# Kernel tuning notes

Measured on AMD Instinct MI355X. Metric: run time of the kernel, lower is better.

The kernel has to match this reference:

```python
import jax, jax.numpy as jnp
import numpy as np

K = 20          # knn neighbors
EPS = 1e-5      # InstanceNorm2d default eps
SLOPE = 0.2     # LeakyReLU negative_slope


def setup_inputs() -> dict:
    key = jax.random.key(0)
    k1, k2 = jax.random.split(key)
    x = jax.random.normal(k1, (4, 3, 8192), dtype=jnp.float32)   # [B, C, N] point cloud
    W = jax.random.normal(k2, (64, 6), dtype=jnp.float32) * 0.05  # 1x1 conv weight [out, 2C], bias=False
    return {"x": x, "W": W}


def reference(x, W):
    B, C, N = x.shape
    # ---- KNN graph: pairwise squared distances + top-k nearest ----
    inner = jnp.einsum('bcn,bcm->bnm', x, x)                 # [B,N,N]
    sq = jnp.sum(x * x, axis=1)                              # [B,N]
    dist = sq[:, :, None] - 2.0 * inner + sq[:, None, :]     # [B,N,N]
    _, idx = jax.lax.top_k(-dist, K)                         # [B,N,K] nearest (incl. self)
    # ---- gather edge features: concat(x_i, x_j - x_i) ----
    xt = jnp.transpose(x, (0, 2, 1))                         # [B,N,C]
    nbr = jax.vmap(lambda pts, i: pts[i])(xt, idx)           # [B,N,K,C]
    ctr = jnp.broadcast_to(xt[:, :, None, :], nbr.shape)     # [B,N,K,C]
    edge = jnp.concatenate([ctr, nbr - ctr], axis=-1)        # [B,N,K,2C]
    # ---- 1x1 conv (no bias) ----
    y = jnp.einsum('bnkc,oc->bonk', edge, W)                 # [B,O,N,K]
    # ---- InstanceNorm2d (affine=False, biased var) ----
    mean = jnp.mean(y, axis=(2, 3), keepdims=True)
    var = jnp.var(y, axis=(2, 3), keepdims=True)
    y = (y - mean) * jax.lax.rsqrt(var + EPS)
    # ---- LeakyReLU(0.2) ----
    y = jnp.where(y >= 0, y, SLOPE * y)
    # ---- max-pool over neighbors ----
    return jnp.max(y, axis=-1)                               # [B,O,N]
```

## Files before the change

### kernel.cpp

```cpp
#include <hip/hip_runtime.h>

#define Nn 8192
#define Bb 4
#define KK 20
#define OO 64
#define EPSF 1e-5f
#define SLOPEF 0.2f

#define NBUCK 56
#define CAP 256
#define BOFF 476
#define CLO 0.00390625f
#define CHI 63.9999961853f
#define XBINS 256
#define XSCALE 25.6f
#define XOFF 5.0f


__global__ __launch_bounds__(1024) void sort_kernel(const float* __restrict__ x,
                                                    float4* __restrict__ sx,
                                                    int* __restrict__ ord,
                                                    int* __restrict__ cumg) {
  __shared__ unsigned hcnt[XBINS];
  __shared__ unsigned base[XBINS];
  __shared__ unsigned char binb[Nn];
  const int b = blockIdx.x;
  const float* xb = x + b * 3 * Nn;
  for (int t = threadIdx.x; t < XBINS; t += 1024) hcnt[t] = 0u;
  __syncthreads();
  for (int j = threadIdx.x; j < Nn; j += 1024) {
    float a0 = xb[j];
    int bin = (int)((a0 + XOFF) * XSCALE);
    bin = bin < 0 ? 0 : (bin > XBINS - 1 ? XBINS - 1 : bin);
    binb[j] = (unsigned char)bin;
    atomicAdd(&hcnt[bin], 1u);
  }
  __syncthreads();
  if (threadIdx.x == 0) {
    unsigned run = 0;
    #pragma unroll 8
    for (int i = 0; i < XBINS; ++i) {
      base[i] = run;
      cumg[b * (XBINS + 1) + i] = (int)run;
      run += hcnt[i];
    }
    cumg[b * (XBINS + 1) + XBINS] = (int)run;
  }
  __syncthreads();
  for (int j = threadIdx.x; j < Nn; j += 1024) {
    float a0 = xb[j], a1 = xb[Nn + j], a2 = xb[2 * Nn + j];
    unsigned slot = atomicAdd(&base[binb[j]], 1u);
    sx[b * Nn + slot] = make_float4(a0, a1, a2, a0 * a0 + a1 * a1 + a2 * a2);
    ord[b * Nn + slot] = j;
  }
}


__global__ __launch_bounds__(256, 8) void knn_kernel(const float4* __restrict__ sx,
                                                     const int* __restrict__ ord,
                                                     const int* __restrict__ cumg,
                                                     int* __restrict__ idx_out) {
  __shared__ unsigned hist[4][64];
  __shared__ unsigned long long cdk[4][CAP];
  __shared__ unsigned ccnt[4];

  const int lane = threadIdx.x & 63;
  const int wid  = threadIdx.x >> 6;
  const int b    = blockIdx.y;
  const int r    = (wid << 11) + blockIdx.x;

  const float4* __restrict__ sxb  = sx + b * Nn;
  const int*    __restrict__ ordb = ord + b * Nn;
  const int*    __restrict__ cumb = cumg + b * (XBINS + 1);
  const float4 me = sxb[r];

  hist[wid][lane] = 0u;
  if (lane == 0) ccnt[wid] = 0u;

  int sub0 = r - 256; sub0 = sub0 < 0 ? 0 : (sub0 > Nn - 512 ? Nn - 512 : sub0);
  #pragma unroll
  for (int i = 0; i < 8; ++i) {
    float4 p = sxb[sub0 + i * 64 + lane];
    float inner = fmaf(p.x, me.x, fmaf(p.y, me.y, p.z * me.z));
    float d  = fmaf(-2.0f, inner, me.w + p.w);
    float dc = __builtin_amdgcn_fmed3f(d, CLO, CHI);
    atomicAdd(&hist[wid][(__float_as_uint(dc) >> 21) - BOFF], 1u);
  }
  unsigned cum = (lane < NBUCK) ? hist[wid][lane] : 0u;
  #pragma unroll
  for (int off = 1; off < 64; off <<= 1) {
    unsigned o = __shfl_up(cum, off);
    if (lane >= off) cum += o;
  }
  int crit = __popcll(__ballot(lane < NBUCK && cum < KK));
  float Tup = (crit >= NBUCK - 1) ? 256.0f
                                  : __uint_as_float((unsigned)(BOFF + crit + 1) << 21);

  float rT = sqrtf(Tup);
  int bn_ = (int)((me.x - rT - 1e-5f + XOFF) * XSCALE);
  bn_ = bn_ < 0 ? 0 : (bn_ > XBINS - 1 ? XBINS - 1 : bn_);
  int rlo = cumb[bn_];
  bn_ = (int)((me.x + rT + 1e-5f + XOFF) * XSCALE);
  bn_ = bn_ < 0 ? 0 : (bn_ > XBINS - 1 ? XBINS - 1 : bn_);
  int rhi = cumb[bn_ + 1];

  for (int j0 = rlo; j0 < rhi; j0 += 256) {
    #pragma unroll
    for (int t = 0; t < 4; ++t) {
      int j = j0 + t * 64 + lane;
      if (j < rhi) {
        float4 p = sxb[j];
        float inner = fmaf(p.x, me.x, fmaf(p.y, me.y, p.z * me.z));
        float d = fmaf(-2.0f, inner, me.w + p.w);
        if (d < Tup) {
          int bb = (int)__float_as_uint(d);
          unsigned sk = (unsigned)(bb ^ ((bb >> 31) | 0x80000000));
          unsigned c = atomicAdd(&ccnt[wid], 1u);
          if (c < CAP)
            cdk[wid][c] = ((unsigned long long)sk << 32) | (unsigned)ordb[j];
        }
      }
    }
  }
  int cnt = (int)ccnt[wid];

  for (int it = 0; cnt > CAP && it < 4; ++it) {
    hist[wid][lane] = 0u;
    const float s56 = 56.0f / Tup;
    for (int j0 = rlo; j0 < rhi; j0 += 64) {
      int j = j0 + lane;
      if (j < rhi) {
        float4 p = sxb[j];
        float inner = fmaf(p.x, me.x, fmaf(p.y, me.y, p.z * me.z));
        float d = fmaf(-2.0f, inner, me.w + p.w);
        int bk = (int)(d * s56);
        if ((unsigned)bk < (unsigned)NBUCK) atomicAdd(&hist[wid][bk], 1u);
      }
    }
    unsigned cum2 = (lane < NBUCK) ? hist[wid][lane] : 0u;
    #pragma unroll
    for (int off = 1; off < 64; off <<= 1) {
      unsigned o = __shfl_up(cum2, off);
      if (lane >= off) cum2 += o;
    }
    int crit2 = __popcll(__ballot(lane < NBUCK && cum2 < KK));
    unsigned cnew = __shfl(cum2, crit2);
    if (cnew <= CAP) {
      if (lane == 0) ccnt[wid] = 0u;
      for (int j0 = rlo; j0 < rhi; j0 += 64) {
        int j = j0 + lane;
        if (j < rhi) {
          float4 p = sxb[j];
          float inner = fmaf(p.x, me.x, fmaf(p.y, me.y, p.z * me.z));
          float d = fmaf(-2.0f, inner, me.w + p.w);
          int bk = (int)(d * s56);
          if (bk <= crit2) {
            int bb = (int)__float_as_uint(d);
            unsigned sk = (unsigned)(bb ^ ((bb >> 31) | 0x80000000));
            unsigned c = atomicAdd(&ccnt[wid], 1u);
            if (c < CAP)
              cdk[wid][c] = ((unsigned long long)sk << 32) | (unsigned)ordb[j];
          }
        }
      }
      cnt = (int)ccnt[wid];
      break;
    }
    Tup = (float)(crit2 + 1) * (Tup / 56.0f);
    rT = sqrtf(Tup);
    bn_ = (int)((me.x - rT - 1e-5f + XOFF) * XSCALE);
    bn_ = bn_ < 0 ? 0 : (bn_ > XBINS - 1 ? XBINS - 1 : bn_);
    rlo = cumb[bn_];
    bn_ = (int)((me.x + rT + 1e-5f + XOFF) * XSCALE);
    bn_ = bn_ < 0 ? 0 : (bn_ > XBINS - 1 ? XBINS - 1 : bn_);
    rhi = cumb[bn_ + 1];
    cnt = (int)cnew;
  }

  const int nOrig = ordb[r];
  int* op = idx_out + (b * Nn + nOrig) * KK;

  if (cnt <= CAP) {
    for (int c = lane; c < cnt; c += 64) {
      unsigned long long key = cdk[wid][c];
      int rank = 0;
      for (int c2 = 0; c2 < cnt; ++c2) rank += (cdk[wid][c2] < key) ? 1 : 0;
      if (rank < KK) op[rank] = (int)(key & 0xFFFFFFFFu);
    }
  } else {
    unsigned long long last = 0ull;
    for (int k = 0; k < KK; ++k) {
      unsigned long long best = ~0ull;
      for (int j0 = rlo; j0 < rhi; j0 += 64) {
        int j = j0 + lane;
        if (j < rhi) {
          float4 p = sxb[j];
          float inner = fmaf(p.x, me.x, fmaf(p.y, me.y, p.z * me.z));
          float d = fmaf(-2.0f, inner, me.w + p.w);
          int bb = (int)__float_as_uint(d);
          unsigned sk = (unsigned)(bb ^ ((bb >> 31) | 0x80000000));
          unsigned long long key = ((unsigned long long)sk << 32) | (unsigned)ordb[j];
          if (key > last && key < best) best = key;
        }
      }
      #pragma unroll
      for (int off = 32; off >= 1; off >>= 1) {
        unsigned lo_ = (unsigned)best, hi_ = (unsigned)(best >> 32);
        unsigned olo = __shfl_xor(lo_, off), ohi = __shfl_xor(hi_, off);
        unsigned long long o = ((unsigned long long)ohi << 32) | olo;
        if (o < best) best = o;
      }
      if (lane == 0) op[k] = (int)(best & 0xFFFFFFFFu);
      last = best;
    }
  }
}


__global__ __launch_bounds__(256) void uv_kernel(const float* __restrict__ x,
                                                 const float* __restrict__ W,
                                                 float* __restrict__ u,
                                                 float* __restrict__ v) {
  int gid = blockIdx.x * 256 + threadIdx.x;
  int o  = gid & 63;
  int bn = gid >> 6;
  int b  = bn >> 13;
  int n  = bn & (Nn - 1);
  const float* xb = x + b * 3 * Nn;
  float x0 = xb[n], x1 = xb[Nn + n], x2 = xb[2 * Nn + n];
  float wa0 = W[o * 6 + 0], wa1 = W[o * 6 + 1], wa2 = W[o * 6 + 2];
  float wb0 = W[o * 6 + 3], wb1 = W[o * 6 + 4], wb2 = W[o * 6 + 5];
  u[gid] = (wa0 - wb0) * x0 + (wa1 - wb1) * x1 + (wa2 - wb2) * x2;
  v[gid] = wb0 * x0 + wb1 * x1 + wb2 * x2;
}


__global__ __launch_bounds__(256) void gather_kernel(const int* __restrict__ idx,
                                                     float* __restrict__ u,
                                                     const float* __restrict__ v,
                                                     float* __restrict__ stats) {
  __shared__ float ls1[4][64], ls2[4][64];
  int b  = blockIdx.y;
  int o  = threadIdx.x & 63;
  int ys = threadIdx.x >> 6;
  const float* vb = v + (size_t)b * Nn * OO;
  float s1 = 0.f, s2 = 0.f;
  for (int i = 0; i < 16; ++i) {
    int n = blockIdx.x * 64 + ys * 16 + i;
    const int* ip = idx + (b * Nn + n) * KK;
    float un = u[(size_t)(b * Nn + n) * OO + o];
    float sv = 0.f, sv2 = 0.f, mv = -__builtin_inff();
    #pragma unroll
    for (int k = 0; k < KK; ++k) {
      int j = ip[k];
      float val = vb[(size_t)j * OO + o];
      sv += val; sv2 += val * val; mv = fmaxf(mv, val);
    }
    u[(size_t)(b * Nn + n) * OO + o] = un + mv;
    s1 += (float)KK * un + sv;
    s2 += (float)KK * un * un + 2.f * un * sv + sv2;
  }
  ls1[ys][o] = s1; ls2[ys][o] = s2;
  __syncthreads();
  if (ys == 0) {
    float t1 = ls1[0][o] + ls1[1][o] + ls1[2][o] + ls1[3][o];
    float t2 = ls2[0][o] + ls2[1][o] + ls2[2][o] + ls2[3][o];
    atomicAdd(&stats[(b * OO + o) * 2 + 0], t1);
    atomicAdd(&stats[(b * OO + o) * 2 + 1], t2);
  }
}


__global__ __launch_bounds__(256) void out_kernel(const float* __restrict__ pm,
                                                  const float* __restrict__ stats,
                                                  float* __restrict__ out) {
  __shared__ float tile[64][65];
  int b  = blockIdx.y;
  int o  = threadIdx.x & 63;
  int ys = threadIdx.x >> 6;
  const float inv_cnt = 1.0f / (float)(Nn * KK);
  float S1 = stats[(b * OO + o) * 2 + 0];
  float S2 = stats[(b * OO + o) * 2 + 1];
  float mean = S1 * inv_cnt;
  float var  = S2 * inv_cnt - mean * mean;
  float istd = rsqrtf(var + EPSF);
  for (int i = 0; i < 16; ++i) {
    int n = blockIdx.x * 64 + ys * 16 + i;
    float val = (pm[(size_t)(b * Nn + n) * OO + o] - mean) * istd;
    val = (val >= 0.f) ? val : SLOPEF * val;
    tile[ys * 16 + i][o] = val;
  }
  __syncthreads();
  int nb = blockIdx.x * 64;
  for (int i = 0; i < 16; ++i) {
    int oo = ys * 16 + i;
    out[(size_t)(b * OO + oo) * Nn + nb + o] = tile[o][oo];
  }
}


extern "C" void kernel_launch(void* const* d_in, const int* in_sizes, int n_in,
                              void* d_out, int out_size, void* d_ws, size_t ws_size,
                              hipStream_t stream) {
  const float* x = (const float*)d_in[0];
  const float* W = (const float*)d_in[1];
  float* out = (float*)d_out;

  char* ws = (char*)d_ws;
  int*    idx   = (int*)ws;
  float*  u     = (float*)(ws + 2621440);
  float*  v     = (float*)(ws + 11010048);
  float*  stats = (float*)(ws + 19398656);
  float4* sx    = (float4*)(ws + 19402752);
  int*    ord   = (int*)(ws + 19927040);
  int*    cumg  = (int*)(ws + 20058112);

  hipMemsetAsync(stats, 0, Bb * OO * 2 * sizeof(float), stream);
  sort_kernel  <<<Bb, 1024, 0, stream>>>(x, sx, ord, cumg);
  uv_kernel    <<<dim3((Bb * Nn * OO) / 256), 256, 0, stream>>>(x, W, u, v);
  knn_kernel   <<<dim3(Nn / 4, Bb), 256, 0, stream>>>(sx, ord, cumg, idx);
  gather_kernel<<<dim3(128, Bb), 256, 0, stream>>>(idx, u, v, stats);
  out_kernel   <<<dim3(128, Bb), 256, 0, stream>>>(u, stats, out);
}
```

Measured before the change: 217.1 us.

## Process four adjacent sorted queries per wavefront sharing candidate loads

Each wavefront now handles four consecutive queries in x-sorted order instead of one. It scans the union of their candidate ranges once, so each loaded point is reused for four distance evaluations, which amortises global loads and loop overhead. The candidate buffer capacity is reduced to fit four per-query buffers in shared memory. In exchange the union range is wider than each query's own range, register pressure rises under the 8-waves launch bound, and the smaller capacity may trigger the slower refinement paths more often.

```diff
diff --git a/kernel.cpp b/kernel.cpp
--- a/kernel.cpp
+++ b/kernel.cpp
@@ -8,7 +8,7 @@
 #define SLOPEF 0.2f
 
 #define NBUCK 56
-#define CAP 256
+#define CAP 120
 #define BOFF 476
 #define CLO 0.00390625f
 #define CHI 63.9999961853f
@@ -60,158 +60,182 @@
                                                      const int* __restrict__ ord,
                                                      const int* __restrict__ cumg,
                                                      int* __restrict__ idx_out) {
-  __shared__ unsigned hist[4][64];
-  __shared__ unsigned long long cdk[4][CAP];
-  __shared__ unsigned ccnt[4];
+  __shared__ unsigned hist[4][4][64];
+  __shared__ unsigned long long cdk[4][4][CAP];
+  __shared__ unsigned ccnt[4][4];
 
   const int lane = threadIdx.x & 63;
   const int wid  = threadIdx.x >> 6;
   const int b    = blockIdx.y;
-  const int r    = (wid << 11) + blockIdx.x;
+  const int g    = (wid << 9) + blockIdx.x;
+  const int r0   = g << 2;
 
   const float4* __restrict__ sxb  = sx + b * Nn;
   const int*    __restrict__ ordb = ord + b * Nn;
   const int*    __restrict__ cumb = cumg + b * (XBINS + 1);
-  const float4 me = sxb[r];
-
-  hist[wid][lane] = 0u;
-  if (lane == 0) ccnt[wid] = 0u;
-
-  int sub0 = r - 256; sub0 = sub0 < 0 ? 0 : (sub0 > Nn - 512 ? Nn - 512 : sub0);
+
+  float4 me[4];
   #pragma unroll
+  for (int q = 0; q < 4; ++q) me[q] = sxb[r0 + q];
+
+  #pragma unroll
+  for (int q = 0; q < 4; ++q) hist[wid][q][lane] = 0u;
+  if (lane < 4) ccnt[wid][lane] = 0u;
+
+  int sub0 = r0 + 2 - 256; sub0 = sub0 < 0 ? 0 : (sub0 > Nn - 512 ? Nn - 512 : sub0);
+  #pragma unroll 2
   for (int i = 0; i < 8; ++i) {
     float4 p = sxb[sub0 + i * 64 + lane];
-    float inner = fmaf(p.x, me.x, fmaf(p.y, me.y, p.z * me.z));
-    float d  = fmaf(-2.0f, inner, me.w + p.w);
-    float dc = __builtin_amdgcn_fmed3f(d, CLO, CHI);
-    atomicAdd(&hist[wid][(__float_as_uint(dc) >> 21) - BOFF], 1u);
-  }
-  unsigned cum = (lane < NBUCK) ? hist[wid][lane] : 0u;
+    #pragma unroll
+    for (int q = 0; q < 4; ++q) {
+      float inner = fmaf(p.x, me[q].x, fmaf(p.y, me[q].y, p.z * me[q].z));
+      float d  = fmaf(-2.0f, inner, me[q].w + p.w);
+      float dc = __builtin_amdgcn_fmed3f(d, CLO, CHI);
+      atomicAdd(&hist[wid][q][(__float_as_uint(dc) >> 21) - BOFF], 1u);
+    }
+  }
+
+  float Tup[4]; int rlo[4], rhi[4];
+  int rloU = Nn, rhiU = 0;
   #pragma unroll
-  for (int off = 1; off < 64; off <<= 1) {
-    unsigned o = __shfl_up(cum, off);
-    if (lane >= off) cum += o;
-  }
-  int crit = __popcll(__ballot(lane < NBUCK && cum < KK));
-  float Tup = (crit >= NBUCK - 1) ? 256.0f
-                                  : __uint_as_float((unsigned)(BOFF + crit + 1) << 21);
-
-  float rT = sqrtf(Tup);
-  int bn_ = (int)((me.x - rT - 1e-5f + XOFF) * XSCALE);
-  bn_ = bn_ < 0 ? 0 : (bn_ > XBINS - 1 ? XBINS - 1 : bn_);
-  int rlo = cumb[bn_];
-  bn_ = (int)((me.x + rT + 1e-5f + XOFF) * XSCALE);
-  bn_ = bn_ < 0 ? 0 : (bn_ > XBINS - 1 ? XBINS - 1 : bn_);
-  int rhi = cumb[bn_ + 1];
-
-  for (int j0 = rlo; j0 < rhi; j0 += 256) {
-    #pragma unroll
-    for (int t = 0; t < 4; ++t) {
-      int j = j0 + t * 64 + lane;
-      if (j < rhi) {
-        float4 p = sxb[j];
-        float inner = fmaf(p.x, me.x, fmaf(p.y, me.y, p.z * me.z));
-        float d = fmaf(-2.0f, inner, me.w + p.w);
-        if (d < Tup) {
-          int bb = (int)__float_as_uint(d);
-          unsigned sk = (unsigned)(bb ^ ((bb >> 31) | 0x80000000));
-          unsigned c = atomicAdd(&ccnt[wid], 1u);
-          if (c < CAP)
-            cdk[wid][c] = ((unsigned long long)sk << 32) | (unsigned)ordb[j];
-        }
-      }
-    }
-  }
-  int cnt = (int)ccnt[wid];
-
-  for (int it = 0; cnt > CAP && it < 4; ++it) {
-    hist[wid][lane] = 0u;
-    const float s56 = 56.0f / Tup;
-    for (int j0 = rlo; j0 < rhi; j0 += 64) {
-      int j = j0 + lane;
-      if (j < rhi) {
-        float4 p = sxb[j];
-        float inner = fmaf(p.x, me.x, fmaf(p.y, me.y, p.z * me.z));
-        float d = fmaf(-2.0f, inner, me.w + p.w);
-        int bk = (int)(d * s56);
-        if ((unsigned)bk < (unsigned)NBUCK) atomicAdd(&hist[wid][bk], 1u);
-      }
-    }
-    unsigned cum2 = (lane < NBUCK) ? hist[wid][lane] : 0u;
+  for (int q = 0; q < 4; ++q) {
+    unsigned cum = (lane < NBUCK) ? hist[wid][q][lane] : 0u;
     #pragma unroll
     for (int off = 1; off < 64; off <<= 1) {
-      unsigned o = __shfl_up(cum2, off);
-      if (lane >= off) cum2 += o;
-    }
-    int crit2 = __popcll(__ballot(lane < NBUCK && cum2 < KK));
-    unsigned cnew = __shfl(cum2, crit2);
-    if (cnew <= CAP) {
-      if (lane == 0) ccnt[wid] = 0u;
-      for (int j0 = rlo; j0 < rhi; j0 += 64) {
-        int j = j0 + lane;
-        if (j < rhi) {
-          float4 p = sxb[j];
-          float inner = fmaf(p.x, me.x, fmaf(p.y, me.y, p.z * me.z));
-          float d = fmaf(-2.0f, inner, me.w + p.w);
-          int bk = (int)(d * s56);
-          if (bk <= crit2) {
+      unsigned o = __shfl_up(cum, off);
+      if (lane >= off) cum += o;
+    }
+    int crit = __popcll(__ballot(lane < NBUCK && cum < KK));
+    Tup[q] = (crit >= NBUCK - 1) ? 256.0f
+                                 : __uint_as_float((unsigned)(BOFF + crit + 1) << 21);
+    float rT = sqrtf(Tup[q]);
+    int bn_ = (int)((me[q].x - rT - 1e-5f + XOFF) * XSCALE);
+    bn_ = bn_ < 0 ? 0 : (bn_ > XBINS - 1 ? XBINS - 1 : bn_);
+    rlo[q] = cumb[bn_];
+    bn_ = (int)((me[q].x + rT + 1e-5f + XOFF) * XSCALE);
+    bn_ = bn_ < 0 ? 0 : (bn_ > XBINS - 1 ? XBINS - 1 : bn_);
+    rhi[q] = cumb[bn_ + 1];
+    rloU = rlo[q] < rloU ? rlo[q] : rloU;
+    rhiU = rhi[q] > rhiU ? rhi[q] : rhiU;
+  }
+
+  for (int j0 = rloU; j0 < rhiU; j0 += 128) {
+    #pragma unroll
+    for (int t = 0; t < 2; ++t) {
+      int j = j0 + t * 64 + lane;
+      if (j < rhiU) {
+        float4 p = sxb[j];
+        #pragma unroll
+        for (int q = 0; q < 4; ++q) {
+          float inner = fmaf(p.x, me[q].x, fmaf(p.y, me[q].y, p.z * me[q].z));
+          float d = fmaf(-2.0f, inner, me[q].w + p.w);
+          if (d < Tup[q]) {
             int bb = (int)__float_as_uint(d);
             unsigned sk = (unsigned)(bb ^ ((bb >> 31) | 0x80000000));
-            unsigned c = atomicAdd(&ccnt[wid], 1u);
+            unsigned c = atomicAdd(&ccnt[wid][q], 1u);
             if (c < CAP)
-              cdk[wid][c] = ((unsigned long long)sk << 32) | (unsigned)ordb[j];
+              cdk[wid][q][c] = ((unsigned long long)sk << 32) | (unsigned)ordb[j];
           }
         }
       }
-      cnt = (int)ccnt[wid];
-      break;
-    }
-    Tup = (float)(crit2 + 1) * (Tup / 56.0f);
-    rT = sqrtf(Tup);
-    bn_ = (int)((me.x - rT - 1e-5f + XOFF) * XSCALE);
-    bn_ = bn_ < 0 ? 0 : (bn_ > XBINS - 1 ? XBINS - 1 : bn_);
-    rlo = cumb[bn_];
-    bn_ = (int)((me.x + rT + 1e-5f + XOFF) * XSCALE);
-    bn_ = bn_ < 0 ? 0 : (bn_ > XBINS - 1 ? XBINS - 1 : bn_);
-    rhi = cumb[bn_ + 1];
-    cnt = (int)cnew;
-  }
-
-  const int nOrig = ordb[r];
-  int* op = idx_out + (b * Nn + nOrig) * KK;
-
-  if (cnt <= CAP) {
-    for (int c = lane; c < cnt; c += 64) {
-      unsigned long long key = cdk[wid][c];
-      int rank = 0;
-      for (int c2 = 0; c2 < cnt; ++c2) rank += (cdk[wid][c2] < key) ? 1 : 0;
-      if (rank < KK) op[rank] = (int)(key & 0xFFFFFFFFu);
-    }
-  } else {
-    unsigned long long last = 0ull;
-    for (int k = 0; k < KK; ++k) {
-      unsigned long long best = ~0ull;
-      for (int j0 = rlo; j0 < rhi; j0 += 64) {
+    }
+  }
+
+  #pragma unroll
+  for (int q = 0; q < 4; ++q) {
+    int cnt = (int)ccnt[wid][q];
+    float TupQ = Tup[q];
+    int rloQ = rlo[q], rhiQ = rhi[q];
+
+    for (int it = 0; cnt > CAP && it < 4; ++it) {
+      hist[wid][q][lane] = 0u;
+      const float s56 = 56.0f / TupQ;
+      for (int j0 = rloQ; j0 < rhiQ; j0 += 64) {
         int j = j0 + lane;
-        if (j < rhi) {
+        if (j < rhiQ) {
           float4 p = sxb[j];
-          float inner = fmaf(p.x, me.x, fmaf(p.y, me.y, p.z * me.z));
-          float d = fmaf(-2.0f, inner, me.w + p.w);
-          int bb = (int)__float_as_uint(d);
-          unsigned sk = (unsigned)(bb ^ ((bb >> 31) | 0x80000000));
-          unsigned long long key = ((unsigned long long)sk << 32) | (unsigned)ordb[j];
-          if (key > last && key < best) best = key;
-        }
-      }
+          float inner = fmaf(p.x, me[q].x, fmaf(p.y, me[q].y, p.z * me[q].z));
+          float d = fmaf(-2.0f, inner, me[q].w + p.w);
+          int bk = (int)(d * s56);
+          if ((unsigned)bk < (unsigned)NBUCK) atomicAdd(&hist[wid][q][bk], 1u);
+        }
+      }
+      unsigned cum2 = (lane < NBUCK) ? hist[wid][q][lane] : 0u;
       #pragma unroll
-      for (int off = 32; off >= 1; off >>= 1) {
-        unsigned lo_ = (unsigned)best, hi_ = (unsigned)(best >> 32);
-        unsigned olo = __shfl_xor(lo_, off), ohi = __shfl_xor(hi_, off);
-        unsigned long long o = ((unsigned long long)ohi << 32) | olo;
-        if (o < best) best = o;
-      }
-      if (lane == 0) op[k] = (int)(best & 0xFFFFFFFFu);
-      last = best;
+      for (int off = 1; off < 64; off <<= 1) {
+        unsigned o = __shfl_up(cum2, off);
+        if (lane >= off) cum2 += o;
+      }
+      int crit2 = __popcll(__ballot(lane < NBUCK && cum2 < KK));
+      unsigned cnew = __shfl(cum2, crit2);
+      if (cnew <= CAP) {
+        if (lane == 0) ccnt[wid][q] = 0u;
+        for (int j0 = rloQ; j0 < rhiQ; j0 += 64) {
+          int j = j0 + lane;
+          if (j < rhiQ) {
+            float4 p = sxb[j];
+            float inner = fmaf(p.x, me[q].x, fmaf(p.y, me[q].y, p.z * me[q].z));
+            float d = fmaf(-2.0f, inner, me[q].w + p.w);
+            int bk = (int)(d * s56);
+            if (bk <= crit2) {
+              int bb = (int)__float_as_uint(d);
+              unsigned sk = (unsigned)(bb ^ ((bb >> 31) | 0x80000000));
+              unsigned c = atomicAdd(&ccnt[wid][q], 1u);
+              if (c < CAP)
+                cdk[wid][q][c] = ((unsigned long long)sk << 32) | (unsigned)ordb[j];
+            }
+          }
+        }
+        cnt = (int)ccnt[wid][q];
+        break;
+      }
+      TupQ = (float)(crit2 + 1) * (TupQ / 56.0f);
+      float rT = sqrtf(TupQ);
+      int bn_ = (int)((me[q].x - rT - 1e-5f + XOFF) * XSCALE);
+      bn_ = bn_ < 0 ? 0 : (bn_ > XBINS - 1 ? XBINS - 1 : bn_);
+      rloQ = cumb[bn_];
+      bn_ = (int)((me[q].x + rT + 1e-5f + XOFF) * XSCALE);
+      bn_ = bn_ < 0 ? 0 : (bn_ > XBINS - 1 ? XBINS - 1 : bn_);
+      rhiQ = cumb[bn_ + 1];
+      cnt = (int)cnew;
+    }
+
+    const int nOrig = ordb[r0 + q];
+    int* op = idx_out + (b * Nn + nOrig) * KK;
+
+    if (cnt <= CAP) {
+      for (int c = lane; c < cnt; c += 64) {
+        unsigned long long key = cdk[wid][q][c];
+        int rank = 0;
+        for (int c2 = 0; c2 < cnt; ++c2) rank += (cdk[wid][q][c2] < key) ? 1 : 0;
+        if (rank < KK) op[rank] = (int)(key & 0xFFFFFFFFu);
+      }
+    } else {
+      unsigned long long last = 0ull;
+      for (int k = 0; k < KK; ++k) {
+        unsigned long long best = ~0ull;
+        for (int j0 = rloQ; j0 < rhiQ; j0 += 64) {
+          int j = j0 + lane;
+          if (j < rhiQ) {
+            float4 p = sxb[j];
+            float inner = fmaf(p.x, me[q].x, fmaf(p.y, me[q].y, p.z * me[q].z));
+            float d = fmaf(-2.0f, inner, me[q].w + p.w);
+            int bb = (int)__float_as_uint(d);
+            unsigned sk = (unsigned)(bb ^ ((bb >> 31) | 0x80000000));
+            unsigned long long key = ((unsigned long long)sk << 32) | (unsigned)ordb[j];
+            if (key > last && key < best) best = key;
+          }
+        }
+        #pragma unroll
+        for (int off = 32; off >= 1; off >>= 1) {
+          unsigned lo_ = (unsigned)best, hi_ = (unsigned)(best >> 32);
+          unsigned olo = __shfl_xor(lo_, off), ohi = __shfl_xor(hi_, off);
+          unsigned long long o = ((unsigned long long)ohi << 32) | olo;
+          if (o < best) best = o;
+        }
+        if (lane == 0) op[k] = (int)(best & 0xFFFFFFFFu);
+        last = best;
+      }
     }
   }
 }
@@ -318,7 +342,7 @@
   hipMemsetAsync(stats, 0, Bb * OO * 2 * sizeof(float), stream);
   sort_kernel  <<<Bb, 1024, 0, stream>>>(x, sx, ord, cumg);
   uv_kernel    <<<dim3((Bb * Nn * OO) / 256), 256, 0, stream>>>(x, W, u, v);
-  knn_kernel   <<<dim3(Nn / 4, Bb), 256, 0, stream>>>(sx, ord, cumg, idx);
+  knn_kernel   <<<dim3(512, Bb), 256, 0, stream>>>(sx, ord, cumg, idx);
   gather_kernel<<<dim3(128, Bb), 256, 0, stream>>>(idx, u, v, stats);
   out_kernel   <<<dim3(128, Bb), 256, 0, stream>>>(u, stats, out);
 }
```

Result: slower. 277.6 us (+27.9%).
